# Kernel tuning notes

Hardware: AMD Instinct MI355X
Metric: run time of the kernel (lower is better)

The kernel has to match this reference:

```python
import jax, jax.numpy as jnp
import numpy as np

B, C_IN, H, W = 4, 256, 64, 64
LATENT = 256


def conv1x1(x, w, b):
    # x: [B, Cin, H, W], w: [Cout, Cin], b: [Cout]
    return jnp.einsum('bchw,oc->bohw', x, w) + b[None, :, None, None]


def setup_inputs() -> dict:
    key = jax.random.key(0)
    ks = jax.random.split(key, 9)
    s_in = 1.0 / np.sqrt(C_IN)
    s_lat = 1.0 / np.sqrt(LATENT)
    return {
        'x': jax.random.normal(ks[0], (B, C_IN, H, W), dtype=jnp.float32),
        'Wq': jax.random.normal(ks[1], (LATENT, C_IN), dtype=jnp.float32) * s_in,
        'bq': jax.random.normal(ks[2], (LATENT,), dtype=jnp.float32) * 0.01,
        'Wk': jax.random.normal(ks[3], (LATENT, C_IN), dtype=jnp.float32) * s_in,
        'bk': jax.random.normal(ks[4], (LATENT,), dtype=jnp.float32) * 0.01,
        'Wv': jax.random.normal(ks[5], (LATENT, C_IN), dtype=jnp.float32) * s_in,
        'bv': jax.random.normal(ks[6], (LATENT,), dtype=jnp.float32) * 0.01,
        'Wo': jax.random.normal(ks[7], (C_IN, LATENT), dtype=jnp.float32) * s_lat,
        'bo': jax.random.normal(ks[8], (C_IN,), dtype=jnp.float32) * 0.01,
    }


def reference(x, Wq, bq, Wk, bk, Wv, bv, Wo, bo):
    b, _, h, w = x.shape
    n = h * w
    q = conv1x1(x, Wq, bq).reshape(b, LATENT, n)  # [B, L, N]
    k = conv1x1(x, Wk, bk).reshape(b, LATENT, n)
    v = conv1x1(x, Wv, bv).reshape(b, LATENT, n)
    scale = jnp.sqrt(jnp.asarray(LATENT, dtype=x.dtype))
    # attention[b, i, j] = sum_c q[b, c, i] * k[b, c, j]
    attn = jnp.einsum('bci,bcj->bij', q, k) / scale
    # faithful to original: softmax over dim=1 (query index i, per column j)
    attn = jax.nn.softmax(attn, axis=1)
    # res[b, c, j] = sum_i v[b, c, i] * attn[b, i, j]
    res = jnp.einsum('bci,bij->bcj', v, attn).reshape(b, LATENT, h, w)
    return conv1x1(res, Wo, bo)
```

## Files before the change

### kernel.cpp

```cpp
#include <hip/hip_runtime.h>

#define B_  4
#define C_  256
#define N_  4096
#define SCALE 0.0625f

typedef short s8v __attribute__((ext_vector_type(8)));
typedef float f4v __attribute__((ext_vector_type(4)));

static __device__ __forceinline__ ushort f2bf(float f) {
  union { float f; uint u; } v; v.f = f;
  return (ushort)((v.u + 0x7FFFu + ((v.u >> 16) & 1u)) >> 16);
}

__global__ __launch_bounds__(256) void xpose_cast(
    const float* __restrict__ x, ushort* __restrict__ x_t)
{
  const int b  = blockIdx.z;
  const int c0 = blockIdx.y * 64;
  const int n0 = blockIdx.x * 64;
  __shared__ float t[64][65];

  const int tc = threadIdx.x >> 4;
  const int tn = (threadIdx.x & 15) * 4;
  #pragma unroll
  for (int cc = 0; cc < 64; cc += 16) {
    float4 v = *(const float4*)(x + (size_t)(b * C_ + c0 + cc + tc) * N_ + n0 + tn);
    t[cc + tc][tn + 0] = v.x;
    t[cc + tc][tn + 1] = v.y;
    t[cc + tc][tn + 2] = v.z;
    t[cc + tc][tn + 3] = v.w;
  }
  __syncthreads();

  const int on = threadIdx.x >> 2;
  const int oc = (threadIdx.x & 3) * 16;
  union { ushort us[16]; uint4 q[2]; } o;
  #pragma unroll
  for (int i = 0; i < 16; ++i) o.us[i] = f2bf(t[oc + i][on]);
  ushort* dst = x_t + (size_t)(b * N_ + n0 + on) * C_ + c0 + oc;
  *(uint4*)dst       = o.q[0];
  *(uint4*)(dst + 8) = o.q[1];
}

__global__ __launch_bounds__(256, 2) void qkv_mfma(
    const ushort* __restrict__ x_t,
    const float* __restrict__ Wq, const float* __restrict__ bq,
    const float* __restrict__ Wk, const float* __restrict__ bk,
    const float* __restrict__ Wv, const float* __restrict__ bv,
    ushort* __restrict__ q_t, ushort* __restrict__ k_t, ushort* __restrict__ v_bf)
{
  const int p = blockIdx.z >> 2;
  const int b = blockIdx.z & 3;
  const float* W  = (p == 0) ? Wq : (p == 1) ? Wk : Wv;
  const float* bi = (p == 0) ? bq : (p == 1) ? bk : bv;
  const int l0    = blockIdx.y * 64;
  const int nseg  = blockIdx.x * 256;

  const int tid  = threadIdx.x;
  const int lane = tid & 63;
  const int wave = tid >> 6;
  const int l16  = lane & 15;
  const int quad = lane >> 4;

  __shared__ __align__(16) ushort s_lds[64 * 264];

  for (int g = tid; g < 4096; g += 256) {
    int row = g >> 6, col4 = (g & 63) * 4;
    float4 wv = *(const float4*)(W + (size_t)(l0 + row) * 256 + col4);
    *(ushort4*)&s_lds[row * 264 + col4] =
        make_ushort4(f2bf(wv.x), f2bf(wv.y), f2bf(wv.z), f2bf(wv.w));
  }
  __syncthreads();

  s8v kw[4][8];
  #pragma unroll
  for (int lt = 0; lt < 4; ++lt)
    #pragma unroll
    for (int cs = 0; cs < 8; ++cs)
      kw[lt][cs] = *(const s8v*)&s_lds[(lt * 16 + l16) * 264 + quad * 8 + cs * 32];

  float bias_l[4];
  #pragma unroll
  for (int lt = 0; lt < 4; ++lt) bias_l[lt] = bi[l0 + lt * 16 + l16];

  __syncthreads();

  for (int it = 0; it < 4; ++it) {
    const int n0 = nseg + it * 64;
    {
      const ushort* xseg = x_t + (size_t)(b * N_ + n0) * C_;
      #pragma unroll
      for (int k = 0; k < 8; ++k) {
        int c = tid + k * 256;
        uint4 d = *(const uint4*)(xseg + (size_t)c * 8);
        *(uint4*)&s_lds[(c >> 5) * 264 + (c & 31) * 8] = d;
      }
    }
    __syncthreads();

    f4v s[4];
    #pragma unroll
    for (int lt = 0; lt < 4; ++lt) s[lt] = (f4v){0.f, 0.f, 0.f, 0.f};
    const ushort* xa_base = s_lds + (wave * 16 + l16) * 264 + quad * 8;
    #pragma unroll
    for (int cs = 0; cs < 8; ++cs) {
      s8v xa = *(const s8v*)(xa_base + cs * 32);
      #pragma unroll
      for (int lt = 0; lt < 4; ++lt)
        s[lt] = __builtin_amdgcn_mfma_f32_16x16x32_bf16(xa, kw[lt][cs], s[lt], 0, 0, 0);
    }

    const int nb = n0 + wave * 16 + quad * 4;
    if (p < 2) {
      ushort* outp = (p == 0) ? q_t : k_t;
      #pragma unroll
      for (int lt = 0; lt < 4; ++lt) {
        const int l = l0 + lt * 16 + l16;
        #pragma unroll
        for (int r = 0; r < 4; ++r)
          outp[(size_t)(b * N_ + nb + r) * C_ + l] = f2bf(s[lt][r] + bias_l[lt]);
      }
    } else {
      #pragma unroll
      for (int lt = 0; lt < 4; ++lt) {
        const int c_out = l0 + lt * 16 + l16;
        *(ushort4*)&v_bf[(size_t)(b * C_ + c_out) * N_ + nb] =
            make_ushort4(f2bf(s[lt][0] + bias_l[lt]), f2bf(s[lt][1] + bias_l[lt]),
                         f2bf(s[lt][2] + bias_l[lt]), f2bf(s[lt][3] + bias_l[lt]));
      }
    }
    __syncthreads();
  }
}

__global__ __launch_bounds__(256, 2) void flash8b(
    const ushort* __restrict__ q_t, const ushort* __restrict__ k_t,
    const ushort* __restrict__ v_bf, ushort* __restrict__ res0,
    ushort* __restrict__ res1, float* __restrict__ den)
{
  const int tid  = threadIdx.x;
  const int lane = tid & 63;
  const int wave = tid >> 6;
  const int l16  = lane & 15;
  const int quad = lane >> 4;
  const int jw    = blockIdx.x * 64;
  const int seg   = blockIdx.y;
  const int ibase = seg * 2048;
  const int b     = blockIdx.z;

  const int wqk_j = wave & 1;
  const int wqk_i = wave >> 1;

  __shared__ __align__(16) ushort q_lds[64 * 264];
  __shared__ __align__(16) ushort p_lds[64 * 72];

  s8v kf[2][8];
  #pragma unroll
  for (int jt = 0; jt < 2; ++jt) {
    const ushort* kp = k_t + (size_t)(b * N_ + jw + wqk_j * 32 + jt * 16 + l16) * C_ + quad * 8;
    #pragma unroll
    for (int cs = 0; cs < 8; ++cs) kf[jt][cs] = *(const s8v*)(kp + cs * 32);
  }

  f4v acc[4][4];
  #pragma unroll
  for (int m = 0; m < 4; ++m)
    #pragma unroll
    for (int t = 0; t < 4; ++t) acc[m][t] = (f4v){0.f, 0.f, 0.f, 0.f};
  float dacc0 = 0.f, dacc1 = 0.f;

  const ushort* vbase0 = v_bf + (size_t)(b * C_ + wave * 64 + l16) * N_ + quad * 8;

  for (int it = 0; it < 32; ++it) {
    const int i0 = ibase + it * 64;

    {
      const ushort* qseg = q_t + ((size_t)(b * N_) + i0) * C_;
      #pragma unroll
      for (int k = 0; k < 8; ++k) {
        int c = tid + k * 256;
        uint4 d = *(const uint4*)(qseg + (size_t)c * 8);
        *(uint4*)&q_lds[(c >> 5) * 264 + (c & 31) * 8] = d;
      }
    }

    s8v av[4][2];
    #pragma unroll
    for (int m = 0; m < 4; ++m)
      #pragma unroll
      for (int ks = 0; ks < 2; ++ks)
        av[m][ks] = *(const s8v*)(vbase0 + (size_t)(m * 16) * N_ + i0 + ks * 32);

    __syncthreads();

    #pragma unroll
    for (int itile = 0; itile < 2; ++itile) {
      const int i_loc = (wqk_i * 2 + itile) * 16;
      f4v s0 = (f4v){0.f, 0.f, 0.f, 0.f};
      f4v s1 = (f4v){0.f, 0.f, 0.f, 0.f};
      const ushort* qa_base = q_lds + (i_loc + l16) * 264 + quad * 8;
      #pragma unroll
      for (int cs = 0; cs < 8; ++cs) {
        s8v qa = *(const s8v*)(qa_base + cs * 32);
        s0 = __builtin_amdgcn_mfma_f32_16x16x32_bf16(qa, kf[0][cs], s0, 0, 0, 0);
        s1 = __builtin_amdgcn_mfma_f32_16x16x32_bf16(qa, kf[1][cs], s1, 0, 0, 0);
      }
      {
        float e0 = __expf(s0[0] * SCALE), e1 = __expf(s0[1] * SCALE);
        float e2 = __expf(s0[2] * SCALE), e3 = __expf(s0[3] * SCALE);
        dacc0 += (e0 + e1) + (e2 + e3);
        *(ushort4*)&p_lds[(wqk_j * 32 + l16) * 72 + i_loc + quad * 4] =
            make_ushort4(f2bf(e0), f2bf(e1), f2bf(e2), f2bf(e3));
      }
      {
        float e0 = __expf(s1[0] * SCALE), e1 = __expf(s1[1] * SCALE);
        float e2 = __expf(s1[2] * SCALE), e3 = __expf(s1[3] * SCALE);
        dacc1 += (e0 + e1) + (e2 + e3);
        *(ushort4*)&p_lds[(wqk_j * 32 + 16 + l16) * 72 + i_loc + quad * 4] =
            make_ushort4(f2bf(e0), f2bf(e1), f2bf(e2), f2bf(e3));
      }
    }

    __syncthreads();

    #pragma unroll
    for (int ks = 0; ks < 2; ++ks) {
      s8v pb[4];
      #pragma unroll
      for (int t = 0; t < 4; ++t)
        pb[t] = *(const s8v*)&p_lds[(t * 16 + l16) * 72 + ks * 32 + quad * 8];
      #pragma unroll
      for (int m = 0; m < 4; ++m)
        #pragma unroll
        for (int t = 0; t < 4; ++t)
          acc[m][t] = __builtin_amdgcn_mfma_f32_16x16x32_bf16(av[m][ks], pb[t], acc[m][t], 0, 0, 0);
    }
  }

  dacc0 += __shfl_xor(dacc0, 16);  dacc0 += __shfl_xor(dacc0, 32);
  dacc1 += __shfl_xor(dacc1, 16);  dacc1 += __shfl_xor(dacc1, 32);
  if (lane < 16) {
    atomicAdd(&den[b * N_ + jw + wqk_j * 32 + lane], dacc0);
    atomicAdd(&den[b * N_ + jw + wqk_j * 32 + 16 + lane], dacc1);
  }

  #pragma unroll
  for (int m = 0; m < 4; ++m) {
    const int c0 = wave * 64 + m * 16 + quad * 4;
    #pragma unroll
    for (int t = 0; t < 4; ++t) {
      *(ushort4*)&q_lds[(t * 16 + l16) * 264 + c0] =
          make_ushort4(f2bf(acc[m][t][0]), f2bf(acc[m][t][1]),
                       f2bf(acc[m][t][2]), f2bf(acc[m][t][3]));
    }
  }
  __syncthreads();
  {
    ushort* rp = (seg ? res1 : res0) + (size_t)(b * N_ + jw) * C_;
    #pragma unroll
    for (int k = 0; k < 8; ++k) {
      int c = tid + k * 256;
      int row = c >> 5, col = (c & 31) * 8;
      uint4 d = *(const uint4*)&q_lds[row * 264 + col];
      *(uint4*)&rp[(size_t)row * C_ + col] = d;
    }
  }
}

__global__ __launch_bounds__(256, 2) void out_mfma(
    const ushort* __restrict__ res0, const ushort* __restrict__ res1,
    const float* __restrict__ Wo, const float* __restrict__ bo,
    const float* __restrict__ den, float* __restrict__ out)
{
  const int b    = blockIdx.z;
  const int co0  = blockIdx.y * 64;
  const int nseg = blockIdx.x * 128;

  const int tid  = threadIdx.x;
  const int lane = tid & 63;
  const int wave = tid >> 6;
  const int l16  = lane & 15;
  const int quad = lane >> 4;

  __shared__ __align__(16) ushort s_lds[64 * 264];

  for (int g = tid; g < 4096; g += 256) {
    int row = g >> 6, col4 = (g & 63) * 4;
    float4 wv = *(const float4*)(Wo + (size_t)(co0 + row) * 256 + col4);
    *(ushort4*)&s_lds[row * 264 + col4] =
        make_ushort4(f2bf(wv.x), f2bf(wv.y), f2bf(wv.z), f2bf(wv.w));
  }
  __syncthreads();

  s8v kw[4][8];
  #pragma unroll
  for (int lt = 0; lt < 4; ++lt)
    #pragma unroll
    for (int cs = 0; cs < 8; ++cs)
      kw[lt][cs] = *(const s8v*)&s_lds[(lt * 16 + l16) * 264 + quad * 8 + cs * 32];

  float bias_l[4];
  #pragma unroll
  for (int lt = 0; lt < 4; ++lt) bias_l[lt] = bo[co0 + lt * 16 + l16];

  __syncthreads();

  for (int it = 0; it < 2; ++it) {
    const int n0 = nseg + it * 64;

    f4v s[4];
    #pragma unroll
    for (int lt = 0; lt < 4; ++lt) s[lt] = (f4v){0.f, 0.f, 0.f, 0.f};

    #pragma unroll
    for (int buf = 0; buf < 2; ++buf) {
      const ushort* rsrc = (buf ? res1 : res0) + (size_t)(b * N_ + n0) * C_;
      #pragma unroll
      for (int k = 0; k < 8; ++k) {
        int c = tid + k * 256;
        uint4 d = *(const uint4*)(rsrc + (size_t)c * 8);
        *(uint4*)&s_lds[(c >> 5) * 264 + (c & 31) * 8] = d;
      }
      __syncthreads();

      const ushort* ra_base = s_lds + (wave * 16 + l16) * 264 + quad * 8;
      #pragma unroll
      for (int cs = 0; cs < 8; ++cs) {
        s8v ra = *(const s8v*)(ra_base + cs * 32);
        #pragma unroll
        for (int lt = 0; lt < 4; ++lt)
          s[lt] = __builtin_amdgcn_mfma_f32_16x16x32_bf16(ra, kw[lt][cs], s[lt], 0, 0, 0);
      }
      __syncthreads();
    }

    const int nb = n0 + wave * 16 + quad * 4;
    float4 dv = *(const float4*)(den + (size_t)b * N_ + nb);
    const float di0 = 1.0f / dv.x, di1 = 1.0f / dv.y, di2 = 1.0f / dv.z, di3 = 1.0f / dv.w;
    #pragma unroll
    for (int lt = 0; lt < 4; ++lt) {
      const int co = co0 + lt * 16 + l16;
      *(float4*)&out[(size_t)(b * C_ + co) * N_ + nb] =
          make_float4(s[lt][0] * di0 + bias_l[lt], s[lt][1] * di1 + bias_l[lt],
                      s[lt][2] * di2 + bias_l[lt], s[lt][3] * di3 + bias_l[lt]);
    }
  }
}

extern "C" void kernel_launch(void* const* d_in, const int* in_sizes, int n_in,
                              void* d_out, int out_size, void* d_ws, size_t ws_size,
                              hipStream_t stream)
{
  const float* x  = (const float*)d_in[0];
  const float* Wq = (const float*)d_in[1];
  const float* bq = (const float*)d_in[2];
  const float* Wk = (const float*)d_in[3];
  const float* bk = (const float*)d_in[4];
  const float* Wv = (const float*)d_in[5];
  const float* bv = (const float*)d_in[6];
  const float* Wo = (const float*)d_in[7];
  const float* bo = (const float*)d_in[8];
  float* out = (float*)d_out;

  char* ws = (char*)d_ws;
  ushort* q_t  = (ushort*)(ws);
  ushort* k_t  = (ushort*)(ws + (size_t)8  * 1024 * 1024);
  ushort* v_bf = (ushort*)(ws + (size_t)16 * 1024 * 1024);
  ushort* res0 = (ushort*)(ws + (size_t)24 * 1024 * 1024);
  ushort* res1 = (ushort*)(ws + (size_t)32 * 1024 * 1024);
  float*  den  = (float*) (ws + (size_t)40 * 1024 * 1024);
  ushort* x_t  = (ushort*)(ws + (size_t)40 * 1024 * 1024 + 65536);

  (void)hipMemsetAsync(den, 0, (size_t)B_ * N_ * sizeof(float), stream);

  xpose_cast<<<dim3(64, 4, 4), dim3(256), 0, stream>>>(x, x_t);
  qkv_mfma <<<dim3(16, 4, 12), dim3(256), 0, stream>>>(x_t, Wq, bq, Wk, bk, Wv, bv, q_t, k_t, v_bf);
  flash8b  <<<dim3(64, 2, 4),  dim3(256), 0, stream>>>(q_t, k_t, v_bf, res0, res1, den);
  out_mfma <<<dim3(32, 4, 4),  dim3(256), 0, stream>>>(res0, res1, Wo, bo, den, out);
}
```

Measured before the change: 209.1 us.

## Split flash attention over four query segments and enlarge QKV projection tiles

The attention kernel now splits the query (softmax) dimension into up to four segments instead of two. The grid doubles to 1024 blocks, which should fill the GPU better, and each block handles half as many iterations. The output projection sums the extra partial result buffers, reusing the x_t workspace for one of them, and falls back to two segments when the workspace is too small. The QKV projection also gives each block twice as many columns, with separate LDS for weights and x, so the weight conversion is amortised over more work; this adds extra partial-buffer traffic and reduces parallelism in that stage.

New measurement: 216.6 us. +3.6%, slower.

```diff
diff --git a/kernel.cpp b/kernel.cpp
--- a/kernel.cpp
+++ b/kernel.cpp
@@ -55,7 +55,7 @@
   const float* W  = (p == 0) ? Wq : (p == 1) ? Wk : Wv;
   const float* bi = (p == 0) ? bq : (p == 1) ? bk : bv;
   const int l0    = blockIdx.y * 64;
-  const int nseg  = blockIdx.x * 256;
+  const int nseg  = blockIdx.x * 512;
 
   const int tid  = threadIdx.x;
   const int lane = tid & 63;
@@ -63,12 +63,13 @@
   const int l16  = lane & 15;
   const int quad = lane >> 4;
 
-  __shared__ __align__(16) ushort s_lds[64 * 264];
+  __shared__ __align__(16) ushort w_lds[64 * 264];
+  __shared__ __align__(16) ushort x_lds[64 * 264];
 
   for (int g = tid; g < 4096; g += 256) {
     int row = g >> 6, col4 = (g & 63) * 4;
     float4 wv = *(const float4*)(W + (size_t)(l0 + row) * 256 + col4);
-    *(ushort4*)&s_lds[row * 264 + col4] =
+    *(ushort4*)&w_lds[row * 264 + col4] =
         make_ushort4(f2bf(wv.x), f2bf(wv.y), f2bf(wv.z), f2bf(wv.w));
   }
   __syncthreads();
@@ -78,15 +79,13 @@
   for (int lt = 0; lt < 4; ++lt)
     #pragma unroll
     for (int cs = 0; cs < 8; ++cs)
-      kw[lt][cs] = *(const s8v*)&s_lds[(lt * 16 + l16) * 264 + quad * 8 + cs * 32];
+      kw[lt][cs] = *(const s8v*)&w_lds[(lt * 16 + l16) * 264 + quad * 8 + cs * 32];
 
   float bias_l[4];
   #pragma unroll
   for (int lt = 0; lt < 4; ++lt) bias_l[lt] = bi[l0 + lt * 16 + l16];
 
-  __syncthreads();
-
-  for (int it = 0; it < 4; ++it) {
+  for (int it = 0; it < 8; ++it) {
     const int n0 = nseg + it * 64;
     {
       const ushort* xseg = x_t + (size_t)(b * N_ + n0) * C_;
@@ -94,7 +93,7 @@
       for (int k = 0; k < 8; ++k) {
         int c = tid + k * 256;
         uint4 d = *(const uint4*)(xseg + (size_t)c * 8);
-        *(uint4*)&s_lds[(c >> 5) * 264 + (c & 31) * 8] = d;
+        *(uint4*)&x_lds[(c >> 5) * 264 + (c & 31) * 8] = d;
       }
     }
     __syncthreads();
@@ -102,7 +101,7 @@
     f4v s[4];
     #pragma unroll
     for (int lt = 0; lt < 4; ++lt) s[lt] = (f4v){0.f, 0.f, 0.f, 0.f};
-    const ushort* xa_base = s_lds + (wave * 16 + l16) * 264 + quad * 8;
+    const ushort* xa_base = x_lds + (wave * 16 + l16) * 264 + quad * 8;
     #pragma unroll
     for (int cs = 0; cs < 8; ++cs) {
       s8v xa = *(const s8v*)(xa_base + cs * 32);
@@ -134,10 +133,12 @@
   }
 }
 
-__global__ __launch_bounds__(256, 2) void flash8b(
+__global__ __launch_bounds__(256, 2) void flash8c(
     const ushort* __restrict__ q_t, const ushort* __restrict__ k_t,
-    const ushort* __restrict__ v_bf, ushort* __restrict__ res0,
-    ushort* __restrict__ res1, float* __restrict__ den)
+    const ushort* __restrict__ v_bf,
+    ushort* __restrict__ r0, ushort* __restrict__ r1,
+    ushort* __restrict__ r2, ushort* __restrict__ r3,
+    float* __restrict__ den, int niter)
 {
   const int tid  = threadIdx.x;
   const int lane = tid & 63;
@@ -146,7 +147,7 @@
   const int quad = lane >> 4;
   const int jw    = blockIdx.x * 64;
   const int seg   = blockIdx.y;
-  const int ibase = seg * 2048;
+  const int ibase = seg * niter * 64;
   const int b     = blockIdx.z;
 
   const int wqk_j = wave & 1;
@@ -172,7 +173,7 @@
 
   const ushort* vbase0 = v_bf + (size_t)(b * C_ + wave * 64 + l16) * N_ + quad * 8;
 
-  for (int it = 0; it < 32; ++it) {
+  for (int it = 0; it < niter; ++it) {
     const int i0 = ibase + it * 64;
 
     {
@@ -257,7 +258,8 @@
   }
   __syncthreads();
   {
-    ushort* rp = (seg ? res1 : res0) + (size_t)(b * N_ + jw) * C_;
+    ushort* rbase = (seg == 0) ? r0 : (seg == 1) ? r1 : (seg == 2) ? r2 : r3;
+    ushort* rp = rbase + (size_t)(b * N_ + jw) * C_;
     #pragma unroll
     for (int k = 0; k < 8; ++k) {
       int c = tid + k * 256;
@@ -269,13 +271,14 @@
 }
 
 __global__ __launch_bounds__(256, 2) void out_mfma(
-    const ushort* __restrict__ res0, const ushort* __restrict__ res1,
-    const float* __restrict__ Wo, const float* __restrict__ bo,
+    const ushort* __restrict__ r0, const ushort* __restrict__ r1,
+    const ushort* __restrict__ r2, const ushort* __restrict__ r3,
+    int nseg, const float* __restrict__ Wo, const float* __restrict__ bo,
     const float* __restrict__ den, float* __restrict__ out)
 {
   const int b    = blockIdx.z;
   const int co0  = blockIdx.y * 64;
-  const int nseg = blockIdx.x * 128;
+  const int nsg  = blockIdx.x * 128;
 
   const int tid  = threadIdx.x;
   const int lane = tid & 63;
@@ -307,15 +310,15 @@
   __syncthreads();
 
   for (int it = 0; it < 2; ++it) {
-    const int n0 = nseg + it * 64;
+    const int n0 = nsg + it * 64;
 
     f4v s[4];
     #pragma unroll
     for (int lt = 0; lt < 4; ++lt) s[lt] = (f4v){0.f, 0.f, 0.f, 0.f};
 
-    #pragma unroll
-    for (int buf = 0; buf < 2; ++buf) {
-      const ushort* rsrc = (buf ? res1 : res0) + (size_t)(b * N_ + n0) * C_;
+    for (int sg = 0; sg < nseg; ++sg) {
+      const ushort* rbase = (sg == 0) ? r0 : (sg == 1) ? r1 : (sg == 2) ? r2 : r3;
+      const ushort* rsrc = rbase + (size_t)(b * N_ + n0) * C_;
       #pragma unroll
       for (int k = 0; k < 8; ++k) {
         int c = tid + k * 256;
@@ -371,11 +374,17 @@
   ushort* res1 = (ushort*)(ws + (size_t)32 * 1024 * 1024);
   float*  den  = (float*) (ws + (size_t)40 * 1024 * 1024);
   ushort* x_t  = (ushort*)(ws + (size_t)40 * 1024 * 1024 + 65536);
+  ushort* res2 = x_t;
+  ushort* res3 = (ushort*)(ws + (size_t)48 * 1024 * 1024 + 65536);
+
+  const size_t need4 = (size_t)56 * 1024 * 1024 + 65536;
+  const int nseg  = (ws_size >= need4) ? 4 : 2;
+  const int niter = 4096 / (64 * nseg);
 
   (void)hipMemsetAsync(den, 0, (size_t)B_ * N_ * sizeof(float), stream);
 
-  xpose_cast<<<dim3(64, 4, 4), dim3(256), 0, stream>>>(x, x_t);
-  qkv_mfma <<<dim3(16, 4, 12), dim3(256), 0, stream>>>(x_t, Wq, bq, Wk, bk, Wv, bv, q_t, k_t, v_bf);
-  flash8b  <<<dim3(64, 2, 4),  dim3(256), 0, stream>>>(q_t, k_t, v_bf, res0, res1, den);
-  out_mfma <<<dim3(32, 4, 4),  dim3(256), 0, stream>>>(res0, res1, Wo, bo, den, out);
-}
+  xpose_cast<<<dim3(64, 4, 4),    dim3(256), 0, stream>>>(x, x_t);
+  qkv_mfma <<<dim3(8, 4, 12),     dim3(256), 0, stream>>>(x_t, Wq, bq, Wk, bk, Wv, bv, q_t, k_t, v_bf);
+  flash8c  <<<dim3(64, nseg, 4),  dim3(256), 0, stream>>>(q_t, k_t, v_bf, res0, res1, res2, res3, den, niter);
+  out_mfma <<<dim3(32, 4, 4),     dim3(256), 0, stream>>>(res0, res1, res2, res3, nseg, Wo, bo, den, out);
+}
```
